# Optimization experiments

Measured on AMD Instinct MI355X. Metric: run time of the kernel, lower is better.

The kernel has to match this reference:

```python
import jax, jax.numpy as jnp
import numpy as np

EMBED_DIM = 1024
NUM_HEADS = 16
HEAD_DIM = EMBED_DIM // NUM_HEADS
SCALING = HEAD_DIM ** -0.5
TGT_LEN = 2048
BSZ = 2


def setup_inputs() -> dict:
    key = jax.random.key(0)
    ks = jax.random.split(key, 8)
    E = EMBED_DIM
    query = jax.random.normal(ks[0], (TGT_LEN, BSZ, E), dtype=jnp.float32)
    k_in = jax.random.normal(ks[1], (TGT_LEN, BSZ, E), dtype=jnp.float32)
    v_in = jax.random.normal(ks[2], (TGT_LEN, BSZ, E), dtype=jnp.float32)
    attn_mask = jnp.zeros((TGT_LEN, TGT_LEN), dtype=jnp.float32)
    key_padding_mask = jnp.zeros((1, TGT_LEN, TGT_LEN), dtype=jnp.int32)
    # torch.nn.Linear params: y = x @ W.T + b
    lim_qkv = 1.0 / np.sqrt(E)
    W_qkv = jax.random.uniform(ks[3], (3 * E, E), minval=-lim_qkv, maxval=lim_qkv, dtype=jnp.float32)
    b_qkv = jax.random.uniform(ks[4], (3 * E,), minval=-lim_qkv, maxval=lim_qkv, dtype=jnp.float32)
    W_out = jax.random.uniform(ks[5], (E, E), minval=-lim_qkv, maxval=lim_qkv, dtype=jnp.float32)
    b_out = jax.random.uniform(ks[6], (E,), minval=-lim_qkv, maxval=lim_qkv, dtype=jnp.float32)
    return {"query": query, "key": k_in, "value": v_in, "attn_mask": attn_mask,
            "key_padding_mask": key_padding_mask, "W_qkv": W_qkv, "b_qkv": b_qkv,
            "W_out": W_out, "b_out": b_out}


def reference(query, key, value, attn_mask, key_padding_mask, W_qkv, b_qkv, W_out, b_out):
    # NOTE: original module ignores `key`/`value` args (self-attn from query only).
    T, B, E = query.shape
    H, hd = NUM_HEADS, HEAD_DIM
    neg_inf = jnp.float32(-jnp.inf)
    qkv = query @ W_qkv.T + b_qkv                       # [T, B, 3E]
    qkv = jnp.transpose(qkv.reshape(T, B * H, 3 * hd), (1, 0, 2))  # [BH, T, 3hd]
    q, k, v = jnp.split(qkv, 3, axis=-1)                # each [BH, T, hd]
    aw = jnp.einsum('btd,bsd->bts', q, k) * SCALING     # [BH, T, T]
    # quirk of original: exact-zero scores become -inf
    aw = jnp.where(aw == 0, neg_inf, aw)
    am = jnp.where(attn_mask == 0, jnp.float32(0.0), attn_mask * jnp.float32(-10000.0))
    aw = aw + am
    aw = jnp.where(jnp.swapaxes(key_padding_mask, -2, -1) == 0, aw, neg_inf)
    aw = jax.nn.softmax(aw, axis=-1)
    # dropout p=0.0 -> identity
    out = aw @ v                                        # [BH, T, hd]
    # faithful to original: transpose(0,1) then reshape(bsz, tgt_len, E)
    out = jnp.swapaxes(out, 0, 1).reshape(B, T, E)      # [B, T, E]
    return out @ W_out.T + b_out
```

## Files before the change

### kernel.cpp

```cpp
#include <hip/hip_runtime.h>
#include <math.h>

#define TLEN 2048
#define EMB 1024
#define QKVD 3072
#define NROWS 4096
#define LOG2E 1.4426950408889634f

typedef unsigned short u16;
typedef unsigned int u32;
using frag_ab = __attribute__((ext_vector_type(8))) short;
using f32x4   = __attribute__((ext_vector_type(4))) float;

__device__ __forceinline__ u16 f2bf(float x) {
    u32 u = __builtin_bit_cast(u32, x);
    u = (u + 0x7FFFu + ((u >> 16) & 1u)) >> 16;
    return (u16)u;
}

__device__ __forceinline__ float bf2f(u16 h) {
    return __builtin_bit_cast(float, (u32)h << 16);
}

__device__ __forceinline__ u32 cvt_pk_bf16(float lo, float hi) {
    u32 r;
    asm("v_cvt_pk_bf16_f32 %0, %1, %2" : "=v"(r) : "v"(lo), "v"(hi));
    return r;
}

__device__ __forceinline__ float exp2_hw(float x) {
    float r;
    asm("v_exp_f32 %0, %1" : "=v"(r) : "v"(x));
    return r;
}

#define GLL16(g, l) __builtin_amdgcn_global_load_lds(                         \
    (const __attribute__((address_space(1))) void*)(g),                       \
    (__attribute__((address_space(3))) void*)(l), 16, 0, 0)

__global__ __launch_bounds__(256)
void prep(const float* __restrict__ qa, const float* __restrict__ wqkv,
          const float* __restrict__ wout, u16* __restrict__ out,
          const float* __restrict__ am, const int* __restrict__ kpm,
          float* __restrict__ cm, int* __restrict__ flags)
{
    __shared__ int kt[64][65];
    __shared__ int s_any;
    const int tid = threadIdx.x;
    const int bid = blockIdx.x;
    if (bid < 4096) {
        int i = (bid * 256 + tid) * 8;
        const float* src;
        int off;
        if (i < 4194304)      { src = qa;   off = i; }
        else if (i < 7340032) { src = wqkv; off = i - 4194304; }
        else                  { src = wout; off = i - 7340032; }
        float4 x = *reinterpret_cast<const float4*>(src + off);
        float4 y = *reinterpret_cast<const float4*>(src + off + 4);
        union { u16 h[8]; uint4 v; } o;
        o.h[0] = f2bf(x.x); o.h[1] = f2bf(x.y); o.h[2] = f2bf(x.z); o.h[3] = f2bf(x.w);
        o.h[4] = f2bf(y.x); o.h[5] = f2bf(y.y); o.h[6] = f2bf(y.z); o.h[7] = f2bf(y.w);
        *reinterpret_cast<uint4*>(out + i) = o.v;
        return;
    }
    const int id2 = bid - 4096;
    const int s0 = (id2 & 31) * 64, t0 = (id2 >> 5) * 64;
    if (tid == 0) s_any = 0;
    #pragma unroll
    for (int u = 0; u < 4; ++u) {
        int idx = u * 256 + tid;
        int r  = idx >> 4;
        int cq = (idx & 15) * 4;
        int4 v = *reinterpret_cast<const int4*>(&kpm[(size_t)(s0 + r) * TLEN + t0 + cq]);
        kt[r][cq + 0] = v.x; kt[r][cq + 1] = v.y; kt[r][cq + 2] = v.z; kt[r][cq + 3] = v.w;
    }
    __syncthreads();
    float rbuf[4][4];
    int myany = 0;
    #pragma unroll
    for (int u = 0; u < 4; ++u) {
        int idx = u * 256 + tid;
        int r  = idx >> 4;
        int cq = (idx & 15) * 4;
        float4 a = *reinterpret_cast<const float4*>(&am[(size_t)(t0 + r) * TLEN + s0 + cq]);
        const float av[4] = {a.x, a.y, a.z, a.w};
        #pragma unroll
        for (int c = 0; c < 4; ++c) {
            float t = (av[c] == 0.0f) ? 0.0f : av[c] * -10000.0f;
            if (kt[cq + c][r] != 0) t = -INFINITY;
            rbuf[u][c] = t * LOG2E;
            myany |= (rbuf[u][c] != 0.0f);
        }
    }
    if (myany) s_any = 1;
    __syncthreads();
    if (s_any) {
        #pragma unroll
        for (int u = 0; u < 4; ++u) {
            int idx = u * 256 + tid;
            int r  = idx >> 4;
            int cq = (idx & 15) * 4;
            *reinterpret_cast<float4*>(&cm[(size_t)(t0 + r) * TLEN + s0 + cq]) =
                make_float4(rbuf[u][0], rbuf[u][1], rbuf[u][2], rbuf[u][3]);
        }
    }
    if (tid == 0) flags[id2] = s_any;
}

template <int OUT_MODE, int NF>
__global__ __launch_bounds__(256)
void gemm_nt_mfma(const u16* __restrict__ A, const u16* __restrict__ B,
                  const float* __restrict__ bias, void* __restrict__ Cp,
                  u16* __restrict__ Vg, int M, int N, int K)
{
    constexpr int BN = NF * 32;
    __shared__ u16 As[128 * 32];
    __shared__ u16 Bs[BN * 32];
    const int tid  = threadIdx.x;
    const int lane = tid & 63;
    const int w    = tid >> 6;
    const int wr   = w >> 1, wc = w & 1;

    const int nbx = N / BN;
    const int id  = blockIdx.x;
    const int lin = (id & 7) * ((int)gridDim.x >> 3) + (id >> 3);
    const int bm = (lin / nbx) * 128, bn = (lin % nbx) * BN;

    f32x4 acc[4][NF];
    #pragma unroll
    for (int i = 0; i < 4; ++i)
        #pragma unroll
        for (int j = 0; j < NF; ++j)
            acc[i][j] = (f32x4){0.f, 0.f, 0.f, 0.f};

    const int srow = tid >> 2;
    const int skel = (tid & 3) * 8;
    const u16* Ag = A + (size_t)(bm + srow) * K + skel;
    const u16* Bg = B + (size_t)(bn + srow % BN) * K + skel;
    u16* Asl = As + srow * 32 + skel;
    u16* Bsl = Bs + (srow % BN) * 32 + skel;

    const int fr = lane & 15;
    const int fk = (lane >> 4) * 8;

    for (int k0 = 0; k0 < K; k0 += 32) {
        GLL16(Ag + k0, Asl);
        GLL16(Ag + (size_t)64 * K + k0, Asl + 64 * 32);
        GLL16(Bg + k0, Bsl);
        if constexpr (NF == 4) GLL16(Bg + (size_t)64 * K + k0, Bsl + 64 * 32);
        __syncthreads();
        frag_ab af[4], bfr[NF];
        #pragma unroll
        for (int mf = 0; mf < 4; ++mf)
            af[mf] = *reinterpret_cast<const frag_ab*>(&As[(wr * 64 + mf * 16 + fr) * 32 + fk]);
        #pragma unroll
        for (int nf = 0; nf < NF; ++nf)
            bfr[nf] = *reinterpret_cast<const frag_ab*>(
                &Bs[(wc * (NF * 16) + nf * 16 + fr) * 32 + fk]);
        #pragma unroll
        for (int mf = 0; mf < 4; ++mf)
            #pragma unroll
            for (int nf = 0; nf < NF; ++nf)
                acc[mf][nf] = __builtin_amdgcn_mfma_f32_16x16x32_bf16(af[mf], bfr[nf], acc[mf][nf], 0, 0, 0);
        __syncthreads();
    }

    const int col0 = bn + wc * (NF * 16) + fr;
    const int row0 = bm + wr * 64 + (lane >> 4) * 4;
    #pragma unroll
    for (int nf = 0; nf < NF; ++nf) {
        const int col = col0 + nf * 16;
        const float bv = bias[col];
        if constexpr (OUT_MODE == 0) {
            #pragma unroll
            for (int mf = 0; mf < 4; ++mf)
                #pragma unroll
                for (int i = 0; i < 4; ++i)
                    ((float*)Cp)[(size_t)(row0 + mf * 16 + i) * N + col] = acc[mf][nf][i] + bv;
        } else {
            const u32 q6 = (u32)col >> 6;
            const u32 h = (q6 * 0xAAABu) >> 17;
            const int seg = col - (int)h * 192;
            if (seg < 128) {
                #pragma unroll
                for (int mf = 0; mf < 4; ++mf)
                    #pragma unroll
                    for (int i = 0; i < 4; ++i)
                        ((u16*)Cp)[(size_t)(row0 + mf * 16 + i) * N + col] =
                            f2bf(acc[mf][nf][i] + bv);
            } else {
                const int d = seg - 128;
                #pragma unroll
                for (int mf = 0; mf < 4; ++mf)
                    #pragma unroll
                    for (int i = 0; i < 4; ++i) {
                        const int row = row0 + mf * 16 + i;
                        Vg[(size_t)(((row & 1) * 16 + (int)h) * 64 + d) * TLEN + (row >> 1)] =
                            f2bf(acc[mf][nf][i] + bv);
                    }
            }
        }
    }
}

#define SM_VT 16384
#define SM_Q  32768

#define ATTN_STEP(CUR, NXT, IT, SLIM, SIN, SOUT)                              \
  {                                                                           \
                    \
    float vq[4][4];                                                           \
    _Pragma("unroll") for (int nf = 0; nf < 4; ++nf) {                        \
      _Pragma("unroll") for (int i = 0; i < 4; ++i) {                         \
        const float sv = SIN[nf][i];                                          \
        const float v = fmaf(SSCALE, sv, -24.0f);                             \
        vq[nf][i] = (sv == 0.0f) ? -INFINITY : v;                             \
      }                                                                       \
    }                                                                         \
    if (fmask & (1u << (IT))) {                                               \
      _Pragma("unroll") for (int nf = 0; nf < 4; ++nf) {                      \
        const float4 c4 = *reinterpret_cast<const float4*>(                   \
            &cm2[(size_t)rq * TLEN + (IT) * 64 + nf * 16 + 4 * fg]);          \
        vq[nf][0] += c4.x; vq[nf][1] += c4.y;                                 \
        vq[nf][2] += c4.z; vq[nf][3] += c4.w;                                 \
      }                                                                       \
    }                                                                         \
    float pv[4][4];                                                           \
    _Pragma("unroll") for (int nf = 0; nf < 4; ++nf) {                        \
      _Pragma("unroll") for (int i = 0; i < 4; ++i)                           \
        pv[nf][i] = exp2_hw(vq[nf][i]);                                       \
    }                                                                         \
    u32 pkA[4], pkB[4];                                                       \
    _Pragma("unroll") for (int nf = 0; nf < 4; ++nf) {                        \
      pkA[nf] = cvt_pk_bf16(pv[nf][0], pv[nf][1]);                            \
      pkB[nf] = cvt_pk_bf16(pv[nf][2], pv[nf][3]);                            \
    }                                                                         \
                      \
    __builtin_amdgcn_s_setprio(1);                                            \
    _Pragma("unroll") for (int ks = 0; ks < 2; ++ks) {                        \
      u32 d0 = pkA[2 * ks], d1 = pkB[2 * ks];                                 \
      u32 s0 = pkA[2 * ks + 1], s1 = pkB[2 * ks + 1];                         \
      asm("v_permlane32_swap_b32 %0, %1" : "+v"(d0), "+v"(s0));               \
      asm("v_permlane32_swap_b32 %0, %1" : "+v"(d1), "+v"(s1));               \
      const u32 sel0 = odd ? d0 : s0;                                         \
      const u32 sel1 = odd ? d1 : s1;                                         \
      const u32 r0_ = __builtin_amdgcn_ds_swizzle(sel0, 0x401F);              \
      const u32 r1_ = __builtin_amdgcn_ds_swizzle(sel1, 0x401F);              \
      union { u32 wq[4]; frag_ab f; } pau;                                    \
      pau.wq[0] = odd ? r0_ : d0;                                             \
      pau.wq[1] = odd ? r1_ : d1;                                             \
      pau.wq[2] = odd ? s0 : r0_;                                             \
      pau.wq[3] = odd ? s1 : r1_;                                             \
      _Pragma("unroll") for (int nf = 0; nf < 4; ++nf) {                      \
        frag_ab bv = *reinterpret_cast<const frag_ab*>(                       \
            smem + SM_VT + (CUR) * 8192 + nf * 2048 + (ks ? kb1 : kb0));      \
        oacc[nf] = __builtin_amdgcn_mfma_f32_16x16x32_bf16(pau.f, bv,         \
                                                           oacc[nf], 0, 0, 0); \
      }                                                                       \
      osum = __builtin_amdgcn_mfma_f32_16x16x32_bf16(pau.f, fones, osum,      \
                                                     0, 0, 0);                \
    }                                                                         \
    __builtin_amdgcn_s_setprio(0);                                            \
    asm volatile("s_waitcnt vmcnt(0)" ::: "memory");                          \
    __builtin_amdgcn_s_barrier();                                             \
          \
    {                                                                         \
      const int itn = ((IT) + 2 < (SLIM)) ? (IT) + 2 : (SLIM) - 1;            \
      GLL16(kbase + (size_t)((itn * 64 + srow) * 2 + b) * QKVD + gsrc,        \
            smem + (CUR) * 8192 + tid * 16);                                  \
      GLL16(vgbase + (size_t)srow * TLEN + itn * 64 + gsrc,                   \
            smem + SM_VT + (CUR) * 8192 + tid * 16);                          \
    }                                                                         \
                          \
    _Pragma("unroll") for (int nf = 0; nf < 4; ++nf)                          \
      SOUT[nf] = (f32x4){0.f, 0.f, 0.f, 0.f};                                 \
    __builtin_amdgcn_s_setprio(1);                                            \
    _Pragma("unroll") for (int nf = 0; nf < 4; ++nf) {                        \
      _Pragma("unroll") for (int ks = 0; ks < 2; ++ks) {                      \
        frag_ab bk = *reinterpret_cast<const frag_ab*>(                       \
            smem + (NXT) * 8192 + nf * 2048 + (ks ? kb1 : kb0));              \
        SOUT[nf] = __builtin_amdgcn_mfma_f32_16x16x32_bf16(bk, aq[ks],        \
                                                           SOUT[nf], 0, 0, 0); \
      }                                                                       \
    }                                                                         \
    __builtin_amdgcn_s_setprio(0);                                            \
  }

template <int NHALF>
__global__ __launch_bounds__(512, 6)
void attn_mfma(const u16* __restrict__ qkv, const float* __restrict__ cm2,
               const int* __restrict__ flags, const u16* __restrict__ Vg,
               u16* __restrict__ X2, u16* __restrict__ opart,
               float* __restrict__ lpart)
{
    __shared__ __attribute__((aligned(16))) char smem[49152];

    const int tid  = threadIdx.x;
    const int lane = tid & 63;
    const int w    = tid >> 6;

    const int id  = blockIdx.x;
    const int cpx = 64 * NHALF;
    const int lin = (id & 7) * cpx + (id >> 3);
    int bh, tt, half;
    if constexpr (NHALF == 2) {
        bh = lin >> 5;  tt = (lin & 31) >> 1;  half = lin & 1;
    } else {
        bh = lin >> 4;  tt = lin & 15;         half = 0;
    }
    const int b = bh >> 4, h = bh & 15;
    const int t0 = tt * 128;
    const int sb = half * (32 / NHALF);
    const int slim = sb + 32 / NHALF;

    const u16* qbase  = qkv + h * 192;
    const u16* kbase  = qkv + h * 192 + 64;
    const u16* vgbase = Vg + (size_t)bh * 64 * TLEN;

    const int srow = tid >> 3;
    const int sgl  = tid & 7;
    const int gsrc = ((sgl ^ (srow & 7)) & 7) * 8;
    const int fr = lane & 15;
    const int fg = lane >> 4;
    const bool odd = (lane & 16) != 0;
    const int rq = t0 + w * 16 + fr;

    const int kb0 = fr * 128 + (((fg) ^ (fr & 7)) & 7) * 16;
    const int kb1 = fr * 128 + (((4 + fg) ^ (fr & 7)) & 7) * 16;

    frag_ab fones;
    #pragma unroll
    for (int j = 0; j < 8; ++j) fones[j] = (short)0x3F80;

    const int* fl = flags + ((t0 >> 6) + (w >> 2)) * 32;
    int fv = 0;
    if (lane < 32) fv = fl[lane];
    const u32 fmask = (u32)__ballot(fv != 0);

    GLL16(qbase + (size_t)((t0 + srow) * 2 + b) * QKVD + gsrc, smem + SM_Q + tid * 16);
    GLL16(qbase + (size_t)((t0 + 64 + srow) * 2 + b) * QKVD + gsrc, smem + SM_Q + 8192 + tid * 16);
    GLL16(kbase + (size_t)((sb * 64 + srow) * 2 + b) * QKVD + gsrc, smem + tid * 16);
    GLL16(vgbase + (size_t)srow * TLEN + sb * 64 + gsrc, smem + SM_VT + tid * 16);
    __syncthreads();

    frag_ab aq[2];
    aq[0] = *reinterpret_cast<const frag_ab*>(smem + SM_Q + w * 2048 + kb0);
    aq[1] = *reinterpret_cast<const frag_ab*>(smem + SM_Q + w * 2048 + kb1);

    GLL16(kbase + (size_t)(((sb + 1) * 64 + srow) * 2 + b) * QKVD + gsrc,
          smem + 8192 + tid * 16);
    GLL16(vgbase + (size_t)srow * TLEN + (sb + 1) * 64 + gsrc,
          smem + SM_VT + 8192 + tid * 16);

    f32x4 oacc[4];
    #pragma unroll
    for (int nf = 0; nf < 4; ++nf) oacc[nf] = (f32x4){0.f, 0.f, 0.f, 0.f};
    f32x4 osum = (f32x4){0.f, 0.f, 0.f, 0.f};
    f32x4 saccA[4], saccB[4];

    const float SSCALE = 0.125f * LOG2E;

    #pragma unroll
    for (int nf = 0; nf < 4; ++nf) saccA[nf] = (f32x4){0.f, 0.f, 0.f, 0.f};
    __builtin_amdgcn_s_setprio(1);
    #pragma unroll
    for (int nf = 0; nf < 4; ++nf) {
        #pragma unroll
        for (int ks = 0; ks < 2; ++ks) {
            frag_ab bk = *reinterpret_cast<const frag_ab*>(
                smem + nf * 2048 + (ks ? kb1 : kb0));
            saccA[nf] = __builtin_amdgcn_mfma_f32_16x16x32_bf16(bk, aq[ks],
                                                                saccA[nf], 0, 0, 0);
        }
    }
    __builtin_amdgcn_s_setprio(0);

    for (int it2 = sb; it2 < slim; it2 += 2) {
        ATTN_STEP(0, 1, it2, slim, saccA, saccB)
        ATTN_STEP(1, 0, it2 + 1, slim, saccB, saccA)
    }

    if constexpr (NHALF == 2) {
        const int pidx = (bh * 16 + tt) * 2 + half;
        u16* ob = opart + (size_t)pidx * 8192;
        #pragma unroll
        for (int i = 0; i < 4; ++i) {
            const int row = w * 16 + fg * 4 + i;
            #pragma unroll
            for (int nf = 0; nf < 4; ++nf)
                ob[row * 64 + nf * 16 + fr] = f2bf(oacc[nf][i]);
            if (fr == 0) lpart[pidx * 128 + row] = osum[i];
        }
    } else {
        #pragma unroll
        for (int i = 0; i < 4; ++i) {
            const int t = t0 + w * 16 + fg * 4 + i;
            const int rout = ((t >= 1024) ? 2048 : 0) + 2 * (t & 1023) + b;
            const float inv = 1.f / osum[i];
            #pragma unroll
            for (int nf = 0; nf < 4; ++nf)
                X2[(size_t)rout * EMB + h * 64 + nf * 16 + fr] = f2bf(oacc[nf][i] * inv);
        }
    }
}

__global__ __launch_bounds__(256)
void combine(const u16* __restrict__ opart, const float* __restrict__ lpart,
             u16* __restrict__ X2)
{
    const int b2 = blockIdx.x;
    const int bh = b2 >> 4, tt = b2 & 15;
    const int b = bh >> 4, h = bh & 15;
    const int tid = threadIdx.x;
    const int r = tid >> 1;
    const int dbase = (tid & 1) * 32;
    const int p0 = (bh * 16 + tt) * 2;
    const u16* o0 = opart + (size_t)p0 * 8192 + r * 64 + dbase;
    const u16* o1 = o0 + 8192;
    const float inv = 1.f / (lpart[p0 * 128 + r] + lpart[(p0 + 1) * 128 + r]);
    const int t = tt * 128 + r;
    const int rout = ((t >= 1024) ? 2048 : 0) + 2 * (t & 1023) + b;
    u16* dst = X2 + (size_t)rout * EMB + h * 64 + dbase;
    #pragma unroll
    for (int j = 0; j < 4; ++j) {
        uint4 a = *reinterpret_cast<const uint4*>(o0 + j * 8);
        uint4 c = *reinterpret_cast<const uint4*>(o1 + j * 8);
        const u32 aw[4] = {a.x, a.y, a.z, a.w};
        const u32 cw[4] = {c.x, c.y, c.z, c.w};
        union { u16 hh[8]; uint4 v; } o;
        #pragma unroll
        for (int k = 0; k < 4; ++k) {
            const float lo = (bf2f((u16)aw[k]) + bf2f((u16)cw[k])) * inv;
            const float hi = (bf2f((u16)(aw[k] >> 16)) + bf2f((u16)(cw[k] >> 16))) * inv;
            o.hh[2 * k]     = f2bf(lo);
            o.hh[2 * k + 1] = f2bf(hi);
        }
        *reinterpret_cast<uint4*>(dst + j * 8) = o.v;
    }
}

extern "C" void kernel_launch(void* const* d_in, const int* in_sizes, int n_in,
                              void* d_out, int out_size, void* d_ws, size_t ws_size,
                              hipStream_t stream)
{
    const float* query = (const float*)d_in[0];
    const float* am    = (const float*)d_in[3];
    const int*   kpm   = (const int*)d_in[4];
    const float* Wqkv  = (const float*)d_in[5];
    const float* bqkv  = (const float*)d_in[6];
    const float* Wout  = (const float*)d_in[7];
    const float* bout  = (const float*)d_in[8];
    float* out = (float*)d_out;

    char* ws = (char*)d_ws;
    u16*   qkv_bf  = (u16*)(ws);
    u16*   x2_bf   = (u16*)(ws + 25165824);
    float* cmask   = (float*)(ws + 33554432);
    u16*   q_bf    = (u16*)(ws + 50331648);
    u16*   wqkv_bf = (u16*)(ws + 58720256);
    u16*   wout_bf = (u16*)(ws + 65011712);
    int*   flags   = (int*)(ws + 67108864);
    u16*   v_tr    = (u16*)(ws + 67112960);
    u16*   opart   = (u16*)(ws + 75501568);
    float* lpart   = (float*)(ws + 92278784);

    const bool split = ws_size >= 92803072u;

    prep<<<5120, 256, 0, stream>>>(query, Wqkv, Wout, q_bf, am, kpm, cmask, flags);

    gemm_nt_mfma<2, 4><<<768, 256, 0, stream>>>(q_bf, wqkv_bf, bqkv, qkv_bf,
                                                v_tr, NROWS, QKVD, EMB);
    if (split) {
        attn_mfma<2><<<1024, 512, 0, stream>>>(qkv_bf, cmask, flags, v_tr,
                                               nullptr, opart, lpart);
        combine<<<512, 256, 0, stream>>>(opart, lpart, x2_bf);
    } else {
        attn_mfma<1><<<512, 512, 0, stream>>>(qkv_bf, cmask, flags, v_tr,
                                              x2_bf, nullptr, nullptr);
    }
    gemm_nt_mfma<0, 2><<<512, 256, 0, stream>>>(x2_bf, wout_bf, bout, out,
                                                nullptr, NROWS, EMB, EMB);
}
```

Before: 137.3 us.

## Fuse split-softmax combine into output GEMM A-load and load Q directly to registers

The separate combine kernel is removed. The output projection GEMM now reads the two partial attention outputs and their row sums, normalizes them and packs the result into the LDS A tile, which removes one launch and the round trip through X2. Attention also loads Q fragments straight from global memory into registers instead of staging them in shared memory. That cuts LDS use from 48KB to 32KB, and the occupancy hint rises from 6 to 8. The catch is that the GEMM A-load becomes synchronous, with VALU conversion work per K step, and it is recomputed redundantly across N tiles.

New measurement: 148.7 us. +8.3%, slower.

```diff
diff --git a/kernel.cpp b/kernel.cpp
--- a/kernel.cpp
+++ b/kernel.cpp
@@ -107,11 +107,12 @@
     if (tid == 0) flags[id2] = s_any;
 }
 
-template <int OUT_MODE, int NF>
+template <int OUT_MODE, int NF, int ACOMB>
 __global__ __launch_bounds__(256)
 void gemm_nt_mfma(const u16* __restrict__ A, const u16* __restrict__ B,
                   const float* __restrict__ bias, void* __restrict__ Cp,
-                  u16* __restrict__ Vg, int M, int N, int K)
+                  u16* __restrict__ Vg, const u16* __restrict__ opart,
+                  const float* __restrict__ lpart, int M, int N, int K)
 {
     constexpr int BN = NF * 32;
     __shared__ u16 As[128 * 32];
@@ -140,12 +141,49 @@
     u16* Asl = As + srow * 32 + skel;
     u16* Bsl = Bs + (srow % BN) * 32 + skel;
 
+    int tt_[2], rowin_[2], b2_[2];
+    if constexpr (ACOMB) {
+        #pragma unroll
+        for (int rr = 0; rr < 2; ++rr) {
+            const int row = bm + rr * 64 + srow;
+            const int t = ((row >= 2048) ? 1024 : 0) + ((row & 2047) >> 1);
+            b2_[rr] = row & 1;
+            tt_[rr] = t >> 7;
+            rowin_[rr] = t & 127;
+        }
+    }
+
     const int fr = lane & 15;
     const int fk = (lane >> 4) * 8;
 
     for (int k0 = 0; k0 < K; k0 += 32) {
-        GLL16(Ag + k0, Asl);
-        GLL16(Ag + (size_t)64 * K + k0, Asl + 64 * 32);
+        if constexpr (ACOMB == 0) {
+            GLL16(Ag + k0, Asl);
+            GLL16(Ag + (size_t)64 * K + k0, Asl + 64 * 32);
+        } else {
+            const int col = k0 + skel;
+            const int hh = col >> 6, d = col & 63;
+            #pragma unroll
+            for (int rr = 0; rr < 2; ++rr) {
+                const int pidx = ((b2_[rr] * 16 + hh) * 16 + tt_[rr]) * 2;
+                const u16* o0 = opart + (size_t)pidx * 8192 + rowin_[rr] * 64 + d;
+                uint4 a4 = *reinterpret_cast<const uint4*>(o0);
+                uint4 c4 = *reinterpret_cast<const uint4*>(o0 + 8192);
+                const float inv = 1.f / (lpart[pidx * 128 + rowin_[rr]] +
+                                         lpart[(pidx + 1) * 128 + rowin_[rr]]);
+                const u32 aw[4] = {a4.x, a4.y, a4.z, a4.w};
+                const u32 cw[4] = {c4.x, c4.y, c4.z, c4.w};
+                u32 pk[4];
+                #pragma unroll
+                for (int kq = 0; kq < 4; ++kq) {
+                    const float lo = (bf2f((u16)aw[kq]) + bf2f((u16)cw[kq])) * inv;
+                    const float hi = (bf2f((u16)(aw[kq] >> 16)) + bf2f((u16)(cw[kq] >> 16))) * inv;
+                    pk[kq] = cvt_pk_bf16(lo, hi);
+                }
+                *reinterpret_cast<uint4*>(Asl + rr * 64 * 32) =
+                    *reinterpret_cast<const uint4*>(pk);
+            }
+        }
         GLL16(Bg + k0, Bsl);
         if constexpr (NF == 4) GLL16(Bg + (size_t)64 * K + k0, Bsl + 64 * 32);
         __syncthreads();
@@ -204,11 +242,9 @@
 }
 
 #define SM_VT 16384
-#define SM_Q  32768
 
 #define ATTN_STEP(CUR, NXT, IT, SLIM, SIN, SOUT)                              \
   {                                                                           \
-                    \
     float vq[4][4];                                                           \
     _Pragma("unroll") for (int nf = 0; nf < 4; ++nf) {                        \
       _Pragma("unroll") for (int i = 0; i < 4; ++i) {                         \
@@ -235,7 +271,6 @@
       pkA[nf] = cvt_pk_bf16(pv[nf][0], pv[nf][1]);                            \
       pkB[nf] = cvt_pk_bf16(pv[nf][2], pv[nf][3]);                            \
     }                                                                         \
-                      \
     __builtin_amdgcn_s_setprio(1);                                            \
     _Pragma("unroll") for (int ks = 0; ks < 2; ++ks) {                        \
       u32 d0 = pkA[2 * ks], d1 = pkB[2 * ks];                                 \
@@ -263,7 +298,6 @@
     __builtin_amdgcn_s_setprio(0);                                            \
     asm volatile("s_waitcnt vmcnt(0)" ::: "memory");                          \
     __builtin_amdgcn_s_barrier();                                             \
-          \
     {                                                                         \
       const int itn = ((IT) + 2 < (SLIM)) ? (IT) + 2 : (SLIM) - 1;            \
       GLL16(kbase + (size_t)((itn * 64 + srow) * 2 + b) * QKVD + gsrc,        \
@@ -271,7 +305,6 @@
       GLL16(vgbase + (size_t)srow * TLEN + itn * 64 + gsrc,                   \
             smem + SM_VT + (CUR) * 8192 + tid * 16);                          \
     }                                                                         \
-                          \
     _Pragma("unroll") for (int nf = 0; nf < 4; ++nf)                          \
       SOUT[nf] = (f32x4){0.f, 0.f, 0.f, 0.f};                                 \
     __builtin_amdgcn_s_setprio(1);                                            \
@@ -287,13 +320,13 @@
   }
 
 template <int NHALF>
-__global__ __launch_bounds__(512, 6)
+__global__ __launch_bounds__(512, 8)
 void attn_mfma(const u16* __restrict__ qkv, const float* __restrict__ cm2,
                const int* __restrict__ flags, const u16* __restrict__ Vg,
                u16* __restrict__ X2, u16* __restrict__ opart,
                float* __restrict__ lpart)
 {
-    __shared__ __attribute__((aligned(16))) char smem[49152];
+    __shared__ __attribute__((aligned(16))) char smem[32768];
 
     const int tid  = threadIdx.x;
     const int lane = tid & 63;
@@ -313,7 +346,6 @@
     const int sb = half * (32 / NHALF);
     const int slim = sb + 32 / NHALF;
 
-    const u16* qbase  = qkv + h * 192;
     const u16* kbase  = qkv + h * 192 + 64;
     const u16* vgbase = Vg + (size_t)bh * 64 * TLEN;
 
@@ -337,20 +369,20 @@
     if (lane < 32) fv = fl[lane];
     const u32 fmask = (u32)__ballot(fv != 0);
 
-    GLL16(qbase + (size_t)((t0 + srow) * 2 + b) * QKVD + gsrc, smem + SM_Q + tid * 16);
-    GLL16(qbase + (size_t)((t0 + 64 + srow) * 2 + b) * QKVD + gsrc, smem + SM_Q + 8192 + tid * 16);
+    frag_ab aq[2];
+    {
+        const u16* qrow = qkv + (size_t)(rq * 2 + b) * QKVD + h * 192;
+        aq[0] = *reinterpret_cast<const frag_ab*>(qrow + fg * 8);
+        aq[1] = *reinterpret_cast<const frag_ab*>(qrow + (4 + fg) * 8);
+    }
+
     GLL16(kbase + (size_t)((sb * 64 + srow) * 2 + b) * QKVD + gsrc, smem + tid * 16);
     GLL16(vgbase + (size_t)srow * TLEN + sb * 64 + gsrc, smem + SM_VT + tid * 16);
-    __syncthreads();
-
-    frag_ab aq[2];
-    aq[0] = *reinterpret_cast<const frag_ab*>(smem + SM_Q + w * 2048 + kb0);
-    aq[1] = *reinterpret_cast<const frag_ab*>(smem + SM_Q + w * 2048 + kb1);
-
     GLL16(kbase + (size_t)(((sb + 1) * 64 + srow) * 2 + b) * QKVD + gsrc,
           smem + 8192 + tid * 16);
     GLL16(vgbase + (size_t)srow * TLEN + (sb + 1) * 64 + gsrc,
           smem + SM_VT + 8192 + tid * 16);
+    __syncthreads();
 
     f32x4 oacc[4];
     #pragma unroll
@@ -401,41 +433,6 @@
             for (int nf = 0; nf < 4; ++nf)
                 X2[(size_t)rout * EMB + h * 64 + nf * 16 + fr] = f2bf(oacc[nf][i] * inv);
         }
-    }
-}
-
-__global__ __launch_bounds__(256)
-void combine(const u16* __restrict__ opart, const float* __restrict__ lpart,
-             u16* __restrict__ X2)
-{
-    const int b2 = blockIdx.x;
-    const int bh = b2 >> 4, tt = b2 & 15;
-    const int b = bh >> 4, h = bh & 15;
-    const int tid = threadIdx.x;
-    const int r = tid >> 1;
-    const int dbase = (tid & 1) * 32;
-    const int p0 = (bh * 16 + tt) * 2;
-    const u16* o0 = opart + (size_t)p0 * 8192 + r * 64 + dbase;
-    const u16* o1 = o0 + 8192;
-    const float inv = 1.f / (lpart[p0 * 128 + r] + lpart[(p0 + 1) * 128 + r]);
-    const int t = tt * 128 + r;
-    const int rout = ((t >= 1024) ? 2048 : 0) + 2 * (t & 1023) + b;
-    u16* dst = X2 + (size_t)rout * EMB + h * 64 + dbase;
-    #pragma unroll
-    for (int j = 0; j < 4; ++j) {
-        uint4 a = *reinterpret_cast<const uint4*>(o0 + j * 8);
-        uint4 c = *reinterpret_cast<const uint4*>(o1 + j * 8);
-        const u32 aw[4] = {a.x, a.y, a.z, a.w};
-        const u32 cw[4] = {c.x, c.y, c.z, c.w};
-        union { u16 hh[8]; uint4 v; } o;
-        #pragma unroll
-        for (int k = 0; k < 4; ++k) {
-            const float lo = (bf2f((u16)aw[k]) + bf2f((u16)cw[k])) * inv;
-            const float hi = (bf2f((u16)(aw[k] >> 16)) + bf2f((u16)(cw[k] >> 16))) * inv;
-            o.hh[2 * k]     = f2bf(lo);
-            o.hh[2 * k + 1] = f2bf(hi);
-        }
-        *reinterpret_cast<uint4*>(dst + j * 8) = o.v;
     }
 }
 
@@ -468,16 +465,20 @@
 
     prep<<<5120, 256, 0, stream>>>(query, Wqkv, Wout, q_bf, am, kpm, cmask, flags);
 
-    gemm_nt_mfma<2, 4><<<768, 256, 0, stream>>>(q_bf, wqkv_bf, bqkv, qkv_bf,
-                                                v_tr, NROWS, QKVD, EMB);
+    gemm_nt_mfma<2, 4, 0><<<768, 256, 0, stream>>>(q_bf, wqkv_bf, bqkv, qkv_bf,
+                                                   v_tr, nullptr, nullptr,
+                                                   NROWS, QKVD, EMB);
     if (split) {
         attn_mfma<2><<<1024, 512, 0, stream>>>(qkv_bf, cmask, flags, v_tr,
                                                nullptr, opart, lpart);
-        combine<<<512, 256, 0, stream>>>(opart, lpart, x2_bf);
+        gemm_nt_mfma<0, 2, 1><<<512, 256, 0, stream>>>(opart, wout_bf, bout, out,
+                                                       nullptr, opart, lpart,
+                                                       NROWS, EMB, EMB);
     } else {
         attn_mfma<1><<<512, 512, 0, stream>>>(qkv_bf, cmask, flags, v_tr,
                                               x2_bf, nullptr, nullptr);
-    }
-    gemm_nt_mfma<0, 2><<<512, 256, 0, stream>>>(x2_bf, wout_bf, bout, out,
-                                                nullptr, NROWS, EMB, EMB);
-}
+        gemm_nt_mfma<0, 2, 0><<<512, 256, 0, stream>>>(x2_bf, wout_bf, bout, out,
+                                                       nullptr, nullptr, nullptr,
+                                                       NROWS, EMB, EMB);
+    }
+}
```
